# Performance work log

Hardware: AMD Instinct MI355X
Metric: run time of the kernel (lower is better)

Reference implementation:

```python
import jax, jax.numpy as jnp
import numpy as np

BINS = 256
H = 2048
N = 2_000_000


def _tensor2image(x):
    # standard GAN denorm: [-1,1] -> [0,1]
    return (x + 1.0) * 0.5


def _cdf(vals):
    # torch.histc(bins=256, min=0, max=256): unit-width bins, values in [0,255]
    idx = jnp.clip(jnp.floor(vals), 0, BINS - 1).astype(jnp.int32)
    hist = jnp.zeros((BINS,), jnp.float32).at[idx].add(1.0)
    return jnp.cumsum(hist) / hist.sum()


def _trans_table(ref_cdf, adj_cdf):
    # cal_trans: for i in 1..255, first j in 1..255 with adj[j-1] <= ref[i] <= adj[j]
    i_vals = ref_cdf[1:]  # [255]
    cond = (adj_cdf[:-1][None, :] <= i_vals[:, None]) & (i_vals[:, None] <= adj_cdf[1:][None, :])  # [255,255]
    found = cond.any(axis=1)
    first_j = jnp.argmax(cond, axis=1) + 1
    tab = jnp.where(found, first_j, jnp.arange(1, BINS))  # unmatched entries keep identity
    tab = jnp.concatenate([jnp.zeros((1,), tab.dtype), tab])
    tab = tab.at[BINS - 1].set(BINS - 1)
    return tab.astype(jnp.float32)


def _hist_match(dst_img, ref_img, i0, i1, i2, i3):
    # dst_img, ref_img: [3,H,W]; indices: [N]
    dst_align = dst_img[:, i0, i1]  # [3,N]
    ref_align = ref_img[:, i2, i3]  # [3,N]
    cdf_dst = jax.vmap(_cdf)(dst_align)  # [3,256]
    cdf_ref = jax.vmap(_cdf)(ref_align)  # [3,256]
    tables = jax.vmap(_trans_table)(cdf_dst, cdf_ref)  # [3,256]
    bins = jnp.clip(dst_align, 0, BINS - 1).astype(jnp.int32)  # int() truncation on [0,255]
    new_align = jnp.take_along_axis(tables, bins, axis=1)  # [3,N]
    return dst_img.at[:, i0, i1].set(new_align)


def reference(input_data, target_data, mask_src, mask_tar, index0, index1, index2, index3, ref_data):
    inp = _tensor2image(input_data) * 255.0
    tgt = _tensor2image(target_data) * 255.0
    ref = _tensor2image(ref_data) * 255.0
    h = mask_src.shape[2]
    m_src = jnp.broadcast_to(mask_src, (1, 3, h, h))
    m_tar = jnp.broadcast_to(mask_tar, (1, 3, h, h))
    input_masked = inp * m_src
    target_masked = (tgt * m_tar)[0]  # [3,H,W]
    ref_masked = (ref * m_src)[0]     # [3,H,W]
    i0, i1, i2, i3 = index0[0], index1[0], index2[0], index3[0]
    matched = _hist_match(ref_masked, target_masked, i0, i1, i2, i3)[None]  # [1,3,H,W]
    input_match = jax.lax.stop_gradient(matched) * m_src  # no_grad in original
    return jnp.mean((input_masked - input_match) ** 2)


def setup_inputs() -> dict:
    key = jax.random.key(0)
    ks = jax.random.split(key, 9)
    inp = {
        "input_data": jax.random.uniform(ks[0], (1, 3, H, H), jnp.float32, -1.0, 1.0),
        "target_data": jax.random.uniform(ks[1], (1, 3, H, H), jnp.float32, -1.0, 1.0),
        "mask_src": (jax.random.uniform(ks[2], (1, 1, H, H)) > 0.5).astype(jnp.float32),
        "mask_tar": (jax.random.uniform(ks[3], (1, 1, H, H)) > 0.5).astype(jnp.float32),
        "index0": jax.random.randint(ks[4], (1, N), 0, H, jnp.int32),
        "index1": jax.random.randint(ks[5], (1, N), 0, H, jnp.int32),
        "index2": jax.random.randint(ks[6], (1, N), 0, H, jnp.int32),
        "index3": jax.random.randint(ks[7], (1, N), 0, H, jnp.int32),
        "ref_data": jax.random.uniform(ks[8], (1, 3, H, H), jnp.float32, -1.0, 1.0),
    }
    return inp
```

## Files before the change

kernel.cpp:

```cpp
#include <hip/hip_runtime.h>

#define HDIM 2048
#define HH (HDIM * HDIM)
#define NIDX 2000000
#define BINS 256
#define NCOPY 16
#define TL_BLOCKS 2048
#define NCHUNK 2000
#define CH_I4 250
#define NWIN 64

#define PART_OFF     0
#define TAB_OFF      16384
#define WGL_OFF      20480
#define HIST_OFF     24576
#define CNT_D_OFF    131072
#define CNT_R_OFF    393216
#define OFF_D_OFF    655360
#define OFF_R_OFF    1179648
#define FLAGS_OFF    2097152
#define SORT_D_OFF   6291456
#define SORT_R_OFF   10485760
#define PACKED_D_OFF 16777216
#define PACKED_R_OFF 33554432

__global__ __launch_bounds__(256) void pack_kernel(
    const float* __restrict__ ref, const float* __restrict__ tgt,
    const float* __restrict__ msrc, const float* __restrict__ mtar,
    const int* __restrict__ i0, const int* __restrict__ i1,
    const int* __restrict__ i2, const int* __restrict__ i3,
    unsigned* __restrict__ packed_d, unsigned* __restrict__ packed_r,
    unsigned* __restrict__ hist, unsigned* __restrict__ flags32,
    unsigned short* __restrict__ cnt_d, unsigned short* __restrict__ cnt_r)
{
    __shared__ unsigned cntd[NWIN], cntr[NWIN];
    const int t = threadIdx.x;
    const int gtid = blockIdx.x * 256 + t;
    const int stride = gridDim.x * 256;

    for (int k = gtid; k < NCOPY * 6 * BINS; k += stride) hist[k] = 0;
    for (int k = gtid; k < HH / 4; k += stride) flags32[k] = 0;

    if (blockIdx.x < NCHUNK) {
        if (t < NWIN) { cntd[t] = 0; cntr[t] = 0; }
        __syncthreads();
        if (t < CH_I4) {
            const int q = blockIdx.x * CH_I4 + t;
            const int4 a = ((const int4*)i0)[q];
            const int4 b = ((const int4*)i1)[q];
            const int4 c = ((const int4*)i2)[q];
            const int4 d = ((const int4*)i3)[q];
            const int pd[4] = {a.x * HDIM + b.x, a.y * HDIM + b.y, a.z * HDIM + b.z, a.w * HDIM + b.w};
            const int pr[4] = {c.x * HDIM + d.x, c.y * HDIM + d.y, c.z * HDIM + d.z, c.w * HDIM + d.w};
#pragma unroll
            for (int k = 0; k < 4; k++) atomicAdd(&cntd[pd[k] >> 16], 1u);
#pragma unroll
            for (int k = 0; k < 4; k++) atomicAdd(&cntr[pr[k] >> 16], 1u);
        }
        __syncthreads();
        if (t < NWIN) {
            cnt_d[blockIdx.x * NWIN + t] = (unsigned short)cntd[t];
            cnt_r[blockIdx.x * NWIN + t] = (unsigned short)cntr[t];
        }
    }

    for (int g = gtid; g < HH / 4; g += stride) {
        const int p = g * 4;
        const float4 ms4 = *(const float4*)(msrc + p);
        const float4 mt4 = *(const float4*)(mtar + p);
        const float ms[4] = {ms4.x, ms4.y, ms4.z, ms4.w};
        const float mt[4] = {mt4.x, mt4.y, mt4.z, mt4.w};
        unsigned od[4] = {0, 0, 0, 0}, orr[4] = {0, 0, 0, 0};
#pragma unroll
        for (int c = 0; c < 3; c++) {
            const float4 rv = *(const float4*)(ref + c * HH + p);
            const float4 tv = *(const float4*)(tgt + c * HH + p);
            const float r[4] = {rv.x, rv.y, rv.z, rv.w};
            const float tt[4] = {tv.x, tv.y, tv.z, tv.w};
#pragma unroll
            for (int k = 0; k < 4; k++) {
                const float vd = ((r[k] + 1.0f) * 0.5f) * 255.0f * ms[k];
                const float vr = ((tt[k] + 1.0f) * 0.5f) * 255.0f * mt[k];
                const unsigned bd = (unsigned)(int)fminf(fmaxf(floorf(vd), 0.0f), 255.0f);
                const unsigned br = (unsigned)(int)fminf(fmaxf(floorf(vr), 0.0f), 255.0f);
                od[k]  |= bd << (8 * c);
                orr[k] |= br << (8 * c);
            }
        }
        *(uint4*)(packed_d + p) = make_uint4(od[0], od[1], od[2], od[3]);
        *(uint4*)(packed_r + p) = make_uint4(orr[0], orr[1], orr[2], orr[3]);
    }
}

__global__ __launch_bounds__(1024) void off_kernel(
    const unsigned short* __restrict__ cnt_d, const unsigned short* __restrict__ cnt_r,
    unsigned* __restrict__ off_d, unsigned* __restrict__ off_r, unsigned* __restrict__ Wg)
{
    __shared__ unsigned psum[16][NWIN];
    __shared__ unsigned segbase[16][NWIN];
    __shared__ unsigned Wl[NWIN + 1];
    const int t = threadIdx.x;
    const int w = t & 63, seg = t >> 6;

    for (int side = 0; side < 2; side++) {
        const unsigned short* cnt = side ? cnt_r : cnt_d;
        unsigned* off = side ? off_r : off_d;
        unsigned s = 0;
        for (int b = seg * 125; b < seg * 125 + 125; b++) s += cnt[b * NWIN + w];
        psum[seg][w] = s;
        __syncthreads();
        if (t < NWIN) {
            unsigned run = 0;
            for (int sg = 0; sg < 16; sg++) { segbase[sg][t] = run; run += psum[sg][t]; }
            unsigned inc = run;
            for (int d = 1; d < 64; d <<= 1) {
                const unsigned y = __shfl_up(inc, d, 64);
                if (t >= d) inc += y;
            }
            Wl[t] = inc - run;
            if (t == 63) Wl[64] = inc;
        }
        __syncthreads();
        unsigned run = Wl[w] + segbase[seg][w];
        for (int b = seg * 125; b < seg * 125 + 125; b++) {
            off[b * NWIN + w] = run;
            run += cnt[b * NWIN + w];
        }
        if (t < NWIN + 1) Wg[side * (NWIN + 1) + t] = Wl[t];
        __syncthreads();
    }
}

__global__ __launch_bounds__(256) void place_kernel(
    const int* __restrict__ i0, const int* __restrict__ i1,
    const int* __restrict__ i2, const int* __restrict__ i3,
    const unsigned* __restrict__ off_d, const unsigned* __restrict__ off_r,
    unsigned short* __restrict__ sorted_d, unsigned short* __restrict__ sorted_r)
{
    __shared__ unsigned cur[NWIN];
    const int b = blockIdx.x;
    const int t = threadIdx.x;

    if (t < NWIN) cur[t] = off_d[b * NWIN + t];
    __syncthreads();
    if (t < CH_I4) {
        const int q = b * CH_I4 + t;
        const int4 a = ((const int4*)i0)[q];
        const int4 bb = ((const int4*)i1)[q];
        const int pd[4] = {a.x * HDIM + bb.x, a.y * HDIM + bb.y, a.z * HDIM + bb.z, a.w * HDIM + bb.w};
#pragma unroll
        for (int k = 0; k < 4; k++) {
            const unsigned pos = atomicAdd(&cur[pd[k] >> 16], 1u);
            sorted_d[pos] = (unsigned short)(pd[k] & 0xFFFF);
        }
    }
    __syncthreads();
    if (t < NWIN) cur[t] = off_r[b * NWIN + t];
    __syncthreads();
    if (t < CH_I4) {
        const int q = b * CH_I4 + t;
        const int4 c = ((const int4*)i2)[q];
        const int4 d = ((const int4*)i3)[q];
        const int pr[4] = {c.x * HDIM + d.x, c.y * HDIM + d.y, c.z * HDIM + d.z, c.w * HDIM + d.w};
#pragma unroll
        for (int k = 0; k < 4; k++) {
            const unsigned pos = atomicAdd(&cur[pr[k] >> 16], 1u);
            sorted_r[pos] = (unsigned short)(pr[k] & 0xFFFF);
        }
    }
}

__global__ __launch_bounds__(256) void whist_kernel(
    const unsigned* __restrict__ packed_d, const unsigned* __restrict__ packed_r,
    const unsigned short* __restrict__ sorted_d, const unsigned short* __restrict__ sorted_r,
    const unsigned* __restrict__ Wg,
    unsigned char* __restrict__ flags, unsigned* __restrict__ hist)
{
    __shared__ unsigned lhist[6 * BINS];
    __shared__ unsigned Ws[NWIN + 1];
    const int t = threadIdx.x;
    for (int k = t; k < 6 * BINS; k += 256) lhist[k] = 0;
    if (t < NWIN + 1) Ws[t] = Wg[t];
    __syncthreads();

    unsigned z0 = 0, z1 = 0, z2 = 0, z3 = 0, z4 = 0, z5 = 0;
    const int stride = gridDim.x * 256;

    for (int q = blockIdx.x * 256 + t; q < NIDX / 4; q += stride) {
        const uint2 sv = ((const uint2*)sorted_d)[q];
        const unsigned lo[4] = {sv.x & 0xFFFFu, sv.x >> 16, sv.y & 0xFFFFu, sv.y >> 16};
        const unsigned e0 = (unsigned)q * 4u;
        int wlo = 0, whi = NWIN;
        while (wlo + 1 < whi) { const int mid = (wlo + whi) >> 1; if (Ws[mid] <= e0) wlo = mid; else whi = mid; }
        int w = wlo;
#pragma unroll
        for (int k = 0; k < 4; k++) {
            const unsigned e = e0 + k;
            while (w < NWIN - 1 && Ws[w + 1] <= e) w++;
            const int pd = (w << 16) | (int)lo[k];
            const unsigned wd = packed_d[pd];
            flags[pd] = 1;
            const unsigned d0 =  wd        & 255u;
            const unsigned d1 = (wd >> 8 ) & 255u;
            const unsigned d2 = (wd >> 16) & 255u;
            if (d0) atomicAdd(&lhist[           d0], 1u); else z0++;
            if (d1) atomicAdd(&lhist[1 * BINS + d1], 1u); else z1++;
            if (d2) atomicAdd(&lhist[2 * BINS + d2], 1u); else z2++;
        }
    }
    __syncthreads();
    if (t < NWIN + 1) Ws[t] = Wg[NWIN + 1 + t];
    __syncthreads();
    for (int q = blockIdx.x * 256 + t; q < NIDX / 4; q += stride) {
        const uint2 sv = ((const uint2*)sorted_r)[q];
        const unsigned lo[4] = {sv.x & 0xFFFFu, sv.x >> 16, sv.y & 0xFFFFu, sv.y >> 16};
        const unsigned e0 = (unsigned)q * 4u;
        int wlo = 0, whi = NWIN;
        while (wlo + 1 < whi) { const int mid = (wlo + whi) >> 1; if (Ws[mid] <= e0) wlo = mid; else whi = mid; }
        int w = wlo;
#pragma unroll
        for (int k = 0; k < 4; k++) {
            const unsigned e = e0 + k;
            while (w < NWIN - 1 && Ws[w + 1] <= e) w++;
            const int pr = (w << 16) | (int)lo[k];
            const unsigned wr = packed_r[pr];
            const unsigned r0 =  wr        & 255u;
            const unsigned r1 = (wr >> 8 ) & 255u;
            const unsigned r2 = (wr >> 16) & 255u;
            if (r0) atomicAdd(&lhist[3 * BINS + r0], 1u); else z3++;
            if (r1) atomicAdd(&lhist[4 * BINS + r1], 1u); else z4++;
            if (r2) atomicAdd(&lhist[5 * BINS + r2], 1u); else z5++;
        }
    }

    if (z0) atomicAdd(&lhist[0 * BINS], z0);
    if (z1) atomicAdd(&lhist[1 * BINS], z1);
    if (z2) atomicAdd(&lhist[2 * BINS], z2);
    if (z3) atomicAdd(&lhist[3 * BINS], z3);
    if (z4) atomicAdd(&lhist[4 * BINS], z4);
    if (z5) atomicAdd(&lhist[5 * BINS], z5);
    __syncthreads();
    unsigned* h = hist + (blockIdx.x & (NCOPY - 1)) * (6 * BINS);
    for (int k = t; k < 6 * BINS; k += 256) {
        const unsigned v = lhist[k];
        if (v) atomicAdd(&h[k], v);
    }
}

__global__ __launch_bounds__(256) void table_kernel(
    const unsigned* __restrict__ hist, float* __restrict__ tabg)
{
    __shared__ float    cdf[6 * BINS];
    __shared__ unsigned wsum[4];

    const int t    = threadIdx.x;
    const int lane = t & 63;
    const int wid  = t >> 6;

    for (int ch = 0; ch < 6; ch++) {
        unsigned x = 0;
#pragma unroll
        for (int cp = 0; cp < NCOPY; cp++) x += hist[cp * (6 * BINS) + ch * BINS + t];
#pragma unroll
        for (int d = 1; d < 64; d <<= 1) {
            const unsigned y = __shfl_up(x, d, 64);
            if (lane >= d) x += y;
        }
        if (lane == 63) wsum[wid] = x;
        __syncthreads();
        unsigned prefix = 0;
        for (int w = 0; w < wid; w++) prefix += wsum[w];
        x += prefix;
        cdf[ch * BINS + t] = (float)x / 2000000.0f;
        __syncthreads();
    }
    for (int c = 0; c < 3; c++) {
        float o;
        if (t == 0)             o = 0.0f;
        else if (t == BINS - 1) o = 255.0f;
        else {
            const float v = cdf[c * BINS + t];
            const float* arr = cdf + (3 + c) * BINS;
            int lo = 0, hi = 256;
            while (lo < hi) { const int mid = (lo + hi) >> 1; if (arr[mid] < v) lo = mid + 1; else hi = mid; }
            const int J0 = ((lo > 1) ? lo : 1) - 1;
            int lo2 = 0, hi2 = 256;
            while (lo2 < hi2) { const int mid = (lo2 + hi2) >> 1; if (arr[mid] <= v) lo2 = mid + 1; else hi2 = mid; }
            const int J1 = ((lo2 - 1) < 254 ? (lo2 - 1) : 254);
            const bool found = (lo2 >= 1) && (J0 <= J1);
            o = found ? (float)(J0 + 1) : (float)t;
        }
        tabg[c * BINS + t] = o;
    }
}

__global__ __launch_bounds__(256) void tabloss_kernel(
    const float* __restrict__ inp, const float* __restrict__ ref,
    const float* __restrict__ msrc, const float* __restrict__ tabg,
    const unsigned char* __restrict__ flags, double* __restrict__ partials)
{
    __shared__ float  tab[3 * BINS];
    __shared__ double red[256];

    const int t = threadIdx.x;
    for (int k = t; k < 3 * BINS; k += 256) tab[k] = tabg[k];
    __syncthreads();

    double local = 0.0;
    const int stride = gridDim.x * 256;
    for (int g = blockIdx.x * 256 + t; g < HH / 4; g += stride) {
        const int p = g * 4;
        const float4 mv = *(const float4*)(msrc + p);
        const uchar4 fw = *(const uchar4*)(flags + p);
        const unsigned samp[4] = {fw.x, fw.y, fw.z, fw.w};
        const float m[4] = {mv.x, mv.y, mv.z, mv.w};
#pragma unroll
        for (int c = 0; c < 3; c++) {
            const float4 rv = *(const float4*)(ref + c * HH + p);
            const float4 iv = *(const float4*)(inp + c * HH + p);
            const float r[4] = {rv.x, rv.y, rv.z, rv.w};
            const float x4[4] = {iv.x, iv.y, iv.z, iv.w};
            float s = 0.0f;
#pragma unroll
            for (int k = 0; k < 4; k++) {
                const float mm = m[k];
                const float refm = ((r[k] + 1.0f) * 0.5f) * 255.0f * mm;
                const float inpm = ((x4[k] + 1.0f) * 0.5f) * 255.0f * mm;
                float matchv;
                if (samp[k]) {
                    const int bidx = (int)fminf(fmaxf(refm, 0.0f), 255.0f);
                    matchv = tab[c * BINS + bidx];
                } else {
                    matchv = refm;
                }
                const float dd = inpm - matchv * mm;
                s += dd * dd;
            }
            local += (double)s;
        }
    }
    red[t] = local;
    __syncthreads();
    for (int s2 = 128; s2 > 0; s2 >>= 1) {
        if (t < s2) red[t] += red[t + s2];
        __syncthreads();
    }
    if (t == 0) partials[blockIdx.x] = red[0];
}

__global__ __launch_bounds__(256) void finalize_kernel(
    const double* __restrict__ partials, float* __restrict__ out)
{
    const int t = threadIdx.x;
    double s = 0.0;
    for (int k = t; k < TL_BLOCKS; k += 256) s += partials[k];
    __shared__ double red[256];
    red[t] = s;
    __syncthreads();
    for (int s2 = 128; s2 > 0; s2 >>= 1) {
        if (t < s2) red[t] += red[t + s2];
        __syncthreads();
    }
    if (t == 0) out[0] = (float)(red[0] / (double)(3 * HH));
}

extern "C" void kernel_launch(void* const* d_in, const int* in_sizes, int n_in,
                              void* d_out, int out_size, void* d_ws, size_t ws_size,
                              hipStream_t stream)
{
    const float* input_data  = (const float*)d_in[0];
    const float* target_data = (const float*)d_in[1];
    const float* mask_src    = (const float*)d_in[2];
    const float* mask_tar    = (const float*)d_in[3];
    const int*   i0          = (const int*)d_in[4];
    const int*   i1          = (const int*)d_in[5];
    const int*   i2          = (const int*)d_in[6];
    const int*   i3          = (const int*)d_in[7];
    const float* ref_data    = (const float*)d_in[8];
    float* out = (float*)d_out;

    char* ws = (char*)d_ws;
    double*         partials = (double*)(ws + PART_OFF);
    float*          tabg     = (float*)(ws + TAB_OFF);
    unsigned*       Wg       = (unsigned*)(ws + WGL_OFF);
    unsigned*       hist     = (unsigned*)(ws + HIST_OFF);
    unsigned short* cnt_d    = (unsigned short*)(ws + CNT_D_OFF);
    unsigned short* cnt_r    = (unsigned short*)(ws + CNT_R_OFF);
    unsigned*       off_d    = (unsigned*)(ws + OFF_D_OFF);
    unsigned*       off_r    = (unsigned*)(ws + OFF_R_OFF);
    unsigned*       flags32  = (unsigned*)(ws + FLAGS_OFF);
    unsigned char*  flags    = (unsigned char*)(ws + FLAGS_OFF);
    unsigned short* sorted_d = (unsigned short*)(ws + SORT_D_OFF);
    unsigned short* sorted_r = (unsigned short*)(ws + SORT_R_OFF);
    unsigned*       packed_d = (unsigned*)(ws + PACKED_D_OFF);
    unsigned*       packed_r = (unsigned*)(ws + PACKED_R_OFF);

    pack_kernel<<<2048, 256, 0, stream>>>(ref_data, target_data, mask_src, mask_tar,
                                          i0, i1, i2, i3,
                                          packed_d, packed_r, hist, flags32, cnt_d, cnt_r);
    off_kernel<<<1, 1024, 0, stream>>>(cnt_d, cnt_r, off_d, off_r, Wg);
    place_kernel<<<NCHUNK, 256, 0, stream>>>(i0, i1, i2, i3, off_d, off_r, sorted_d, sorted_r);
    whist_kernel<<<2048, 256, 0, stream>>>(packed_d, packed_r, sorted_d, sorted_r, Wg,
                                           flags, hist);
    table_kernel<<<1, 256, 0, stream>>>(hist, tabg);
    tabloss_kernel<<<TL_BLOCKS, 256, 0, stream>>>(input_data, ref_data, mask_src, tabg,
                                                  flags, partials);
    finalize_kernel<<<1, 256, 0, stream>>>(partials, out);
}
```

Baseline: 385.4 us.

## Drop dense pack pass; gather raw pixels by window in histogram kernel

Removes the full-image pre-pass that read all ref/target channels and masks and wrote packed 8-bit bins for every pixel. The histogram kernel now reads the raw float channels and mask only at the sampled, window-sorted positions and computes the bins there. Work is also reassigned so each block owns a class of 64K windows and strides through that window's sorted entries, which replaces the per-element binary search over window boundaries. This avoids a dense read-and-write of about 100MB, at the cost of four scattered float gathers per sample instead of one packed word.

```diff
diff --git a/kernel.cpp b/kernel.cpp
--- a/kernel.cpp
+++ b/kernel.cpp
@@ -10,26 +10,21 @@
 #define CH_I4 250
 #define NWIN 64
 
-#define PART_OFF     0
-#define TAB_OFF      16384
-#define WGL_OFF      20480
-#define HIST_OFF     24576
-#define CNT_D_OFF    131072
-#define CNT_R_OFF    393216
-#define OFF_D_OFF    655360
-#define OFF_R_OFF    1179648
-#define FLAGS_OFF    2097152
-#define SORT_D_OFF   6291456
-#define SORT_R_OFF   10485760
-#define PACKED_D_OFF 16777216
-#define PACKED_R_OFF 33554432
-
-__global__ __launch_bounds__(256) void pack_kernel(
-    const float* __restrict__ ref, const float* __restrict__ tgt,
-    const float* __restrict__ msrc, const float* __restrict__ mtar,
+#define PART_OFF   0
+#define TAB_OFF    16384
+#define WGL_OFF    20480
+#define HIST_OFF   24576
+#define CNT_D_OFF  131072
+#define CNT_R_OFF  393216
+#define OFF_D_OFF  655360
+#define OFF_R_OFF  1179648
+#define FLAGS_OFF  2097152
+#define SORT_D_OFF 6291456
+#define SORT_R_OFF 10485760
+
+__global__ __launch_bounds__(256) void prep_kernel(
     const int* __restrict__ i0, const int* __restrict__ i1,
     const int* __restrict__ i2, const int* __restrict__ i3,
-    unsigned* __restrict__ packed_d, unsigned* __restrict__ packed_r,
     unsigned* __restrict__ hist, unsigned* __restrict__ flags32,
     unsigned short* __restrict__ cnt_d, unsigned short* __restrict__ cnt_r)
 {
@@ -62,33 +57,6 @@
             cnt_d[blockIdx.x * NWIN + t] = (unsigned short)cntd[t];
             cnt_r[blockIdx.x * NWIN + t] = (unsigned short)cntr[t];
         }
-    }
-
-    for (int g = gtid; g < HH / 4; g += stride) {
-        const int p = g * 4;
-        const float4 ms4 = *(const float4*)(msrc + p);
-        const float4 mt4 = *(const float4*)(mtar + p);
-        const float ms[4] = {ms4.x, ms4.y, ms4.z, ms4.w};
-        const float mt[4] = {mt4.x, mt4.y, mt4.z, mt4.w};
-        unsigned od[4] = {0, 0, 0, 0}, orr[4] = {0, 0, 0, 0};
-#pragma unroll
-        for (int c = 0; c < 3; c++) {
-            const float4 rv = *(const float4*)(ref + c * HH + p);
-            const float4 tv = *(const float4*)(tgt + c * HH + p);
-            const float r[4] = {rv.x, rv.y, rv.z, rv.w};
-            const float tt[4] = {tv.x, tv.y, tv.z, tv.w};
-#pragma unroll
-            for (int k = 0; k < 4; k++) {
-                const float vd = ((r[k] + 1.0f) * 0.5f) * 255.0f * ms[k];
-                const float vr = ((tt[k] + 1.0f) * 0.5f) * 255.0f * mt[k];
-                const unsigned bd = (unsigned)(int)fminf(fmaxf(floorf(vd), 0.0f), 255.0f);
-                const unsigned br = (unsigned)(int)fminf(fmaxf(floorf(vr), 0.0f), 255.0f);
-                od[k]  |= bd << (8 * c);
-                orr[k] |= br << (8 * c);
-            }
-        }
-        *(uint4*)(packed_d + p) = make_uint4(od[0], od[1], od[2], od[3]);
-        *(uint4*)(packed_r + p) = make_uint4(orr[0], orr[1], orr[2], orr[3]);
     }
 }
 
@@ -171,65 +139,59 @@
 }
 
 __global__ __launch_bounds__(256) void whist_kernel(
-    const unsigned* __restrict__ packed_d, const unsigned* __restrict__ packed_r,
+    const float* __restrict__ ref, const float* __restrict__ tgt,
+    const float* __restrict__ msrc, const float* __restrict__ mtar,
     const unsigned short* __restrict__ sorted_d, const unsigned short* __restrict__ sorted_r,
     const unsigned* __restrict__ Wg,
     unsigned char* __restrict__ flags, unsigned* __restrict__ hist)
 {
     __shared__ unsigned lhist[6 * BINS];
-    __shared__ unsigned Ws[NWIN + 1];
+    __shared__ unsigned Ws[2 * (NWIN + 1)];
     const int t = threadIdx.x;
     for (int k = t; k < 6 * BINS; k += 256) lhist[k] = 0;
-    if (t < NWIN + 1) Ws[t] = Wg[t];
+    if (t < 2 * (NWIN + 1)) Ws[t] = Wg[t];
     __syncthreads();
 
     unsigned z0 = 0, z1 = 0, z2 = 0, z3 = 0, z4 = 0, z5 = 0;
-    const int stride = gridDim.x * 256;
-
-    for (int q = blockIdx.x * 256 + t; q < NIDX / 4; q += stride) {
-        const uint2 sv = ((const uint2*)sorted_d)[q];
-        const unsigned lo[4] = {sv.x & 0xFFFFu, sv.x >> 16, sv.y & 0xFFFFu, sv.y >> 16};
-        const unsigned e0 = (unsigned)q * 4u;
-        int wlo = 0, whi = NWIN;
-        while (wlo + 1 < whi) { const int mid = (wlo + whi) >> 1; if (Ws[mid] <= e0) wlo = mid; else whi = mid; }
-        int w = wlo;
-#pragma unroll
-        for (int k = 0; k < 4; k++) {
-            const unsigned e = e0 + k;
-            while (w < NWIN - 1 && Ws[w + 1] <= e) w++;
-            const int pd = (w << 16) | (int)lo[k];
-            const unsigned wd = packed_d[pd];
+    const int cls = blockIdx.x & 7;
+    const int bc  = blockIdx.x >> 3;
+    const int cstep = 256 * 256;
+
+    for (int w = cls; w < NWIN; w += 8) {
+        const int base = w << 16;
+        const int e0 = (int)Ws[w], e1 = (int)Ws[w + 1];
+        for (int e = e0 + bc * 256 + t; e < e1; e += cstep) {
+            const int pd = base | (int)sorted_d[e];
+            const float mm = msrc[pd];
+            const float v0 = ref[pd], v1 = ref[HH + pd], v2 = ref[2 * HH + pd];
             flags[pd] = 1;
-            const unsigned d0 =  wd        & 255u;
-            const unsigned d1 = (wd >> 8 ) & 255u;
-            const unsigned d2 = (wd >> 16) & 255u;
-            if (d0) atomicAdd(&lhist[           d0], 1u); else z0++;
-            if (d1) atomicAdd(&lhist[1 * BINS + d1], 1u); else z1++;
-            if (d2) atomicAdd(&lhist[2 * BINS + d2], 1u); else z2++;
-        }
-    }
-    __syncthreads();
-    if (t < NWIN + 1) Ws[t] = Wg[NWIN + 1 + t];
-    __syncthreads();
-    for (int q = blockIdx.x * 256 + t; q < NIDX / 4; q += stride) {
-        const uint2 sv = ((const uint2*)sorted_r)[q];
-        const unsigned lo[4] = {sv.x & 0xFFFFu, sv.x >> 16, sv.y & 0xFFFFu, sv.y >> 16};
-        const unsigned e0 = (unsigned)q * 4u;
-        int wlo = 0, whi = NWIN;
-        while (wlo + 1 < whi) { const int mid = (wlo + whi) >> 1; if (Ws[mid] <= e0) wlo = mid; else whi = mid; }
-        int w = wlo;
-#pragma unroll
-        for (int k = 0; k < 4; k++) {
-            const unsigned e = e0 + k;
-            while (w < NWIN - 1 && Ws[w + 1] <= e) w++;
-            const int pr = (w << 16) | (int)lo[k];
-            const unsigned wr = packed_r[pr];
-            const unsigned r0 =  wr        & 255u;
-            const unsigned r1 = (wr >> 8 ) & 255u;
-            const unsigned r2 = (wr >> 16) & 255u;
-            if (r0) atomicAdd(&lhist[3 * BINS + r0], 1u); else z3++;
-            if (r1) atomicAdd(&lhist[4 * BINS + r1], 1u); else z4++;
-            if (r2) atomicAdd(&lhist[5 * BINS + r2], 1u); else z5++;
+            const float f0 = ((v0 + 1.0f) * 0.5f) * 255.0f * mm;
+            const float f1 = ((v1 + 1.0f) * 0.5f) * 255.0f * mm;
+            const float f2 = ((v2 + 1.0f) * 0.5f) * 255.0f * mm;
+            const unsigned b0 = (unsigned)(int)fminf(fmaxf(floorf(f0), 0.0f), 255.0f);
+            const unsigned b1 = (unsigned)(int)fminf(fmaxf(floorf(f1), 0.0f), 255.0f);
+            const unsigned b2 = (unsigned)(int)fminf(fmaxf(floorf(f2), 0.0f), 255.0f);
+            if (b0) atomicAdd(&lhist[           b0], 1u); else z0++;
+            if (b1) atomicAdd(&lhist[1 * BINS + b1], 1u); else z1++;
+            if (b2) atomicAdd(&lhist[2 * BINS + b2], 1u); else z2++;
+        }
+    }
+    for (int w = cls; w < NWIN; w += 8) {
+        const int base = w << 16;
+        const int e0 = (int)Ws[NWIN + 1 + w], e1 = (int)Ws[NWIN + 1 + w + 1];
+        for (int e = e0 + bc * 256 + t; e < e1; e += cstep) {
+            const int pr = base | (int)sorted_r[e];
+            const float mm = mtar[pr];
+            const float v0 = tgt[pr], v1 = tgt[HH + pr], v2 = tgt[2 * HH + pr];
+            const float f0 = ((v0 + 1.0f) * 0.5f) * 255.0f * mm;
+            const float f1 = ((v1 + 1.0f) * 0.5f) * 255.0f * mm;
+            const float f2 = ((v2 + 1.0f) * 0.5f) * 255.0f * mm;
+            const unsigned b0 = (unsigned)(int)fminf(fmaxf(floorf(f0), 0.0f), 255.0f);
+            const unsigned b1 = (unsigned)(int)fminf(fmaxf(floorf(f1), 0.0f), 255.0f);
+            const unsigned b2 = (unsigned)(int)fminf(fmaxf(floorf(f2), 0.0f), 255.0f);
+            if (b0) atomicAdd(&lhist[3 * BINS + b0], 1u); else z3++;
+            if (b1) atomicAdd(&lhist[4 * BINS + b1], 1u); else z4++;
+            if (b2) atomicAdd(&lhist[5 * BINS + b2], 1u); else z5++;
         }
     }
 
@@ -392,16 +354,12 @@
     unsigned char*  flags    = (unsigned char*)(ws + FLAGS_OFF);
     unsigned short* sorted_d = (unsigned short*)(ws + SORT_D_OFF);
     unsigned short* sorted_r = (unsigned short*)(ws + SORT_R_OFF);
-    unsigned*       packed_d = (unsigned*)(ws + PACKED_D_OFF);
-    unsigned*       packed_r = (unsigned*)(ws + PACKED_R_OFF);
-
-    pack_kernel<<<2048, 256, 0, stream>>>(ref_data, target_data, mask_src, mask_tar,
-                                          i0, i1, i2, i3,
-                                          packed_d, packed_r, hist, flags32, cnt_d, cnt_r);
+
+    prep_kernel<<<2048, 256, 0, stream>>>(i0, i1, i2, i3, hist, flags32, cnt_d, cnt_r);
     off_kernel<<<1, 1024, 0, stream>>>(cnt_d, cnt_r, off_d, off_r, Wg);
     place_kernel<<<NCHUNK, 256, 0, stream>>>(i0, i1, i2, i3, off_d, off_r, sorted_d, sorted_r);
-    whist_kernel<<<2048, 256, 0, stream>>>(packed_d, packed_r, sorted_d, sorted_r, Wg,
-                                           flags, hist);
+    whist_kernel<<<2048, 256, 0, stream>>>(ref_data, target_data, mask_src, mask_tar,
+                                           sorted_d, sorted_r, Wg, flags, hist);
     table_kernel<<<1, 256, 0, stream>>>(hist, tabg);
     tabloss_kernel<<<TL_BLOCKS, 256, 0, stream>>>(input_data, ref_data, mask_src, tabg,
                                                   flags, partials);
```

Result: slower. 395.3 us (+2.6%).
